# Kernel optimization log

Hardware: AMD Instinct MI355X
Metric: run time of the kernel (lower is better)

Reference implementation:

```python
import jax, jax.numpy as jnp
import numpy as np

N = 100000   # nodes
E = 1600000  # edges (avg degree 16)
D = 128      # feature width (in_feats == all hidden_feats)
G = 1024     # number of graphs for global_add_pool
L = 3        # layers
BN_EPS = 1e-5


def setup_inputs() -> dict:
    key = jax.random.key(0)
    ks = jax.random.split(key, 6)
    x = jax.random.normal(ks[0], (N, D), dtype=jnp.float32)
    edge_index = jax.random.randint(ks[1], (2, E), 0, N, dtype=jnp.int32)
    batch = jnp.sort(jax.random.randint(ks[2], (N,), 0, G, dtype=jnp.int32))
    scale = np.float32(1.0 / np.sqrt(D))
    Ws = jax.random.normal(ks[3], (L, D, D), dtype=jnp.float32) * scale   # GCNConv weights
    bs = jnp.zeros((L, D), dtype=jnp.float32)                             # GCNConv biases
    rWs = jax.random.normal(ks[4], (L, D, D), dtype=jnp.float32) * scale  # residual Linear weights
    rbs = jnp.zeros((L, D), dtype=jnp.float32)                            # residual Linear biases
    gammas = jnp.ones((L, D), dtype=jnp.float32)                          # BN affine
    betas = jnp.zeros((L, D), dtype=jnp.float32)
    return {"x": x, "edge_index": edge_index, "batch": batch,
            "Ws": Ws, "bs": bs, "rWs": rWs, "rbs": rbs,
            "gammas": gammas, "betas": betas}


def reference(x, edge_index, batch, Ws, bs, rWs, rbs, gammas, betas):
    src, dst = edge_index[0], edge_index[1]
    # normalize='False' is a truthy string in the original -> PyG GCN norm with self-loops
    loops = jnp.arange(N, dtype=src.dtype)
    src_sl = jnp.concatenate([src, loops])  # [E+N]
    dst_sl = jnp.concatenate([dst, loops])
    deg = jax.ops.segment_sum(jnp.ones(E + N, x.dtype), dst_sl, num_segments=N)
    dinv = jax.lax.rsqrt(deg)  # deg >= 1 thanks to self-loops
    norm = (dinv[src_sl] * dinv[dst_sl])[:, None]  # [E+N, 1]

    for i in range(L):
        h = x @ Ws[i]                                   # [N, D]
        msg = h[src_sl] * norm                          # gather + scale  [E+N, D]
        agg = jax.ops.segment_sum(msg, dst_sl, num_segments=N) + bs[i]
        res = jax.nn.relu(x @ rWs[i] + rbs[i])          # residual linear + ReLU
        h = agg + res
        # BatchNorm1d in training mode: batch stats (biased variance)
        mean = h.mean(axis=0)
        var = h.var(axis=0)
        x = gammas[i] * (h - mean) * jax.lax.rsqrt(var + BN_EPS) + betas[i]

    # global_add_pool over graph ids
    return jax.ops.segment_sum(x, batch, num_segments=G)  # [G, D]
```

## Files before the change

### kernel.cpp

```cpp
#include <hip/hip_runtime.h>

#define D 128
#define NLAYERS 3
#define BN_EPS 1e-5f

typedef short bf16x8 __attribute__((ext_vector_type(8)));
typedef float f32x4 __attribute__((ext_vector_type(4)));

__device__ __forceinline__ unsigned short f2bf(float f) {
    unsigned int u = __float_as_uint(f);
    u += 0x7FFFu + ((u >> 16) & 1u);
    return (unsigned short)(u >> 16);
}
__device__ __forceinline__ float bf2f(unsigned short b) {
    return __uint_as_float(((unsigned int)b) << 16);
}
__device__ __forceinline__ float bf_lo(unsigned int u) {
    return __uint_as_float(u << 16);
}
__device__ __forceinline__ float bf_hi(unsigned int u) {
    return __uint_as_float(u & 0xFFFF0000u);
}


__global__ void k_hist_edges(const int* __restrict__ dst, int* __restrict__ cnt, int E) {
    int i = blockIdx.x * blockDim.x + threadIdx.x;
    if (i < E) atomicAdd(&cnt[dst[i]], 1);
}

__global__ void k_hist_batch(const int* __restrict__ batch, int* __restrict__ gcnt, int N) {
    int i = blockIdx.x * blockDim.x + threadIdx.x;
    if (i < N) atomicAdd(&gcnt[batch[i]], 1);
}

__global__ void k_dinv(const int* __restrict__ cnt, float* __restrict__ dinv, int N) {
    int i = blockIdx.x * blockDim.x + threadIdx.x;
    if (i < N) dinv[i] = rsqrtf((float)(cnt[i] + 1));
}

__global__ void k_csr_init(int* __restrict__ csr, int n, int N) {
    int i = blockIdx.x * blockDim.x + threadIdx.x;
    if (i < n) csr[i] = N;
}

__global__ void k_zrow(unsigned short* __restrict__ hb, int N) {
    hb[(size_t)N * D + threadIdx.x] = 0;
}

__global__ void k_xb(const float* __restrict__ x, unsigned short* __restrict__ fb, int n8) {
    int i = blockIdx.x * blockDim.x + threadIdx.x;
    if (i < n8) {
        const float4 a = ((const float4*)x)[i * 2];
        const float4 b = ((const float4*)x)[i * 2 + 1];
        uint4 p;
        p.x = (unsigned int)f2bf(a.x) | ((unsigned int)f2bf(a.y) << 16);
        p.y = (unsigned int)f2bf(a.z) | ((unsigned int)f2bf(a.w) << 16);
        p.z = (unsigned int)f2bf(b.x) | ((unsigned int)f2bf(b.y) << 16);
        p.w = (unsigned int)f2bf(b.z) | ((unsigned int)f2bf(b.w) << 16);
        ((uint4*)fb)[i] = p;
    }
}

__global__ void k_scan_partial(const int* __restrict__ cnt, int* __restrict__ bsum, int N) {
    __shared__ int sh[256];
    int b = blockIdx.x, t = threadIdx.x;
    int base = b * 1024 + t * 4;
    int s = 0;
#pragma unroll
    for (int i = 0; i < 4; ++i) {
        int idx = base + i;
        int cv = (idx < N) ? cnt[idx] : 0;
        s += (cv + 3) & ~3;
    }
    sh[t] = s;
    for (int ofs = 128; ofs > 0; ofs >>= 1) {
        __syncthreads();
        if (t < ofs) sh[t] += sh[t + ofs];
    }
    __syncthreads();
    if (t == 0) bsum[b] = sh[0];
}

__global__ void k_scan_small(const int* __restrict__ bsum, int* __restrict__ bbase, int nb) {
    __shared__ int sh[256];
    int t = threadIdx.x;
    int v = (t < nb) ? bsum[t] : 0;
    sh[t] = v;
    __syncthreads();
    for (int ofs = 1; ofs < 256; ofs <<= 1) {
        int vv = (t >= ofs) ? sh[t - ofs] : 0;
        __syncthreads();
        sh[t] += vv;
        __syncthreads();
    }
    bbase[t] = sh[t] - v;
}

__global__ void k_scan_apply(const int* __restrict__ cnt, const int* __restrict__ bbase,
                             int* __restrict__ roff, int* __restrict__ cur, int N) {
    __shared__ int sh[256];
    int b = blockIdx.x, t = threadIdx.x;
    int base = b * 1024 + t * 4;
    int v[4]; int s = 0;
#pragma unroll
    for (int i = 0; i < 4; ++i) {
        int cv = (base + i < N) ? cnt[base + i] : 0;
        v[i] = (cv + 3) & ~3;
        s += v[i];
    }
    sh[t] = s;
    __syncthreads();
    for (int ofs = 1; ofs < 256; ofs <<= 1) {
        int vv = (t >= ofs) ? sh[t - ofs] : 0;
        __syncthreads();
        sh[t] += vv;
        __syncthreads();
    }
    int o = bbase[b] + sh[t] - s;
#pragma unroll
    for (int i = 0; i < 4; ++i) {
        int idx = base + i;
        if (idx < N) {
            roff[idx] = o; cur[idx] = o;
            o += v[i];
            if (idx == N - 1) roff[N] = o;
        }
    }
}

__global__ void k_gscan(const int* __restrict__ gcnt, int* __restrict__ goff, int G, int N) {
    __shared__ int sh[256];
    int t = threadIdx.x;
    int base = t * 4;
    int v[4]; int s = 0;
#pragma unroll
    for (int i = 0; i < 4; ++i) { v[i] = (base + i < G) ? gcnt[base + i] : 0; s += v[i]; }
    sh[t] = s;
    __syncthreads();
    for (int ofs = 1; ofs < 256; ofs <<= 1) {
        int vv = (t >= ofs) ? sh[t - ofs] : 0;
        __syncthreads();
        sh[t] += vv;
        __syncthreads();
    }
    int o = sh[t] - s;
#pragma unroll
    for (int i = 0; i < 4; ++i) {
        int idx = base + i;
        if (idx < G) { goff[idx] = o; o += v[i]; }
    }
    if (t == 255) goff[G] = N;
}

__global__ void k_fill(const int* __restrict__ src, const int* __restrict__ dst,
                       int* __restrict__ cur, int* __restrict__ csr, int E) {
    int i = blockIdx.x * blockDim.x + threadIdx.x;
    if (i < E) {
        int p = atomicAdd(&cur[dst[i]], 1);
        csr[p] = src[i];
    }
}

__global__ void k_init_ac(float* __restrict__ a, float* __restrict__ c) {
    int t = threadIdx.x;
    a[t] = 1.0f; c[t] = 0.0f;
}

__global__ void k_packfold(const float* __restrict__ W, const float* __restrict__ rW,
                           const float* __restrict__ a, const float* __restrict__ c,
                           const float* __restrict__ rb,
                           unsigned short* __restrict__ Wp,
                           float* __restrict__ cwA, float* __restrict__ crb) {
    if (blockIdx.x < 128) {
        int idx = blockIdx.x * 256 + threadIdx.x;
        int m = idx >> 14;
        int i = idx & 16383;
        int k = i >> 7, col = i & 127;
        const float* src = m ? rW : W;
        float v = a[k] * src[i];
        int frag = ((k >> 5) << 3) + (col >> 4);
        int lane = (((k & 31) >> 3) << 4) + (col & 15);
        int j = k & 7;
        Wp[(m << 14) + frag * 512 + lane * 8 + j] = f2bf(v);
    } else {
        int t = threadIdx.x;
        if (t < D) {
            float s = 0.f;
            for (int k = 0; k < D; ++k) s += c[k] * W[k * D + t];
            cwA[t] = s;
        } else {
            int j = t - D;
            float s = rb[j];
            for (int k = 0; k < D; ++k) s += c[k] * rW[k * D + j];
            crb[j] = s;
        }
    }
}

__global__ __launch_bounds__(256) void k_gemm_mfma(
    const unsigned short* __restrict__ fb,
    const unsigned short* __restrict__ Wp,
    const float* __restrict__ add0, const float* __restrict__ add1,
    const float* __restrict__ dinv,
    unsigned short* __restrict__ hb, unsigned short* __restrict__ rbuf, int N) {
    __shared__ unsigned short As[128 * 128];
    __shared__ unsigned short Wb[128 * 128];
    const int t = threadIdx.x;
    const int rowbase = blockIdx.x * 128;

#pragma unroll
    for (int i = 0; i < 8; ++i) {
        int ch = t + i * 256;
        int row = ch >> 4, slot = ch & 15;
        uint4 v = make_uint4(0, 0, 0, 0);
        int gr = rowbase + row;
        if (gr < N) v = *(const uint4*)(fb + (size_t)gr * D + slot * 8);
        *(uint4*)((char*)As + row * 256 + ((slot ^ (row & 7)) << 4)) = v;
    }

    const int wave = t >> 6, l = t & 63;
    const int wrow = wave * 32;
    const int lg = l >> 4, lc = l & 15;

    const int g0 = rowbase + wrow + lc;
    const int g1 = g0 + 16;
    const int f0 = lg * 4;

#pragma unroll 1
    for (int m = 0; m < 2; ++m) {
        const unsigned short* wp = Wp + (m << 14);
        __syncthreads();
#pragma unroll
        for (int i = 0; i < 8; ++i) {
            int ch = t + i * 256;
            *(uint4*)((char*)Wb + ch * 16) = *(const uint4*)((const char*)wp + ch * 16);
        }
        __syncthreads();

        f32x4 acc[2][8];
#pragma unroll
        for (int nf = 0; nf < 2; ++nf)
#pragma unroll
            for (int cf = 0; cf < 8; ++cf) acc[nf][cf] = (f32x4){0.f, 0.f, 0.f, 0.f};

#pragma unroll
        for (int ks = 0; ks < 4; ++ks) {
            const int r0 = wrow + lc;
            const int r1 = wrow + 16 + lc;
            const int s = ks * 4 + lg;
            bf16x8 a0 = *(const bf16x8*)((const char*)As + r0 * 256 + ((s ^ (r0 & 7)) << 4));
            bf16x8 a1 = *(const bf16x8*)((const char*)As + r1 * 256 + ((s ^ (r1 & 7)) << 4));
#pragma unroll
            for (int cf = 0; cf < 8; ++cf) {
                bf16x8 b = *(const bf16x8*)((const char*)Wb + ((ks * 8 + cf) * 64 + l) * 16);
                acc[0][cf] = __builtin_amdgcn_mfma_f32_16x16x32_bf16(b, a0, acc[0][cf], 0, 0, 0);
                acc[1][cf] = __builtin_amdgcn_mfma_f32_16x16x32_bf16(b, a1, acc[1][cf], 0, 0, 0);
            }
        }

        if (m == 0) {
            const float dv0 = (g0 < N) ? dinv[g0] : 0.f;
            const float dv1 = (g1 < N) ? dinv[g1] : 0.f;
#pragma unroll
            for (int cf = 0; cf < 8; ++cf) {
                const int fx = cf * 16 + f0;
                const float4 va = *(const float4*)(add0 + fx);
                if (g0 < N) {
                    uint2 p;
                    p.x = (unsigned int)f2bf((acc[0][cf][0] + va.x) * dv0) |
                          ((unsigned int)f2bf((acc[0][cf][1] + va.y) * dv0) << 16);
                    p.y = (unsigned int)f2bf((acc[0][cf][2] + va.z) * dv0) |
                          ((unsigned int)f2bf((acc[0][cf][3] + va.w) * dv0) << 16);
                    *(uint2*)(hb + (size_t)g0 * D + fx) = p;
                }
                if (g1 < N) {
                    uint2 p;
                    p.x = (unsigned int)f2bf((acc[1][cf][0] + va.x) * dv1) |
                          ((unsigned int)f2bf((acc[1][cf][1] + va.y) * dv1) << 16);
                    p.y = (unsigned int)f2bf((acc[1][cf][2] + va.z) * dv1) |
                          ((unsigned int)f2bf((acc[1][cf][3] + va.w) * dv1) << 16);
                    *(uint2*)(hb + (size_t)g1 * D + fx) = p;
                }
            }
        } else {
#pragma unroll
            for (int cf = 0; cf < 8; ++cf) {
                const int fx = cf * 16 + f0;
                const float4 va = *(const float4*)(add1 + fx);
                if (g0 < N) {
                    uint2 p;
                    p.x = (unsigned int)f2bf(fmaxf(acc[0][cf][0] + va.x, 0.f)) |
                          ((unsigned int)f2bf(fmaxf(acc[0][cf][1] + va.y, 0.f)) << 16);
                    p.y = (unsigned int)f2bf(fmaxf(acc[0][cf][2] + va.z, 0.f)) |
                          ((unsigned int)f2bf(fmaxf(acc[0][cf][3] + va.w, 0.f)) << 16);
                    *(uint2*)(rbuf + (size_t)g0 * D + fx) = p;
                }
                if (g1 < N) {
                    uint2 p;
                    p.x = (unsigned int)f2bf(fmaxf(acc[1][cf][0] + va.x, 0.f)) |
                          ((unsigned int)f2bf(fmaxf(acc[1][cf][1] + va.y, 0.f)) << 16);
                    p.y = (unsigned int)f2bf(fmaxf(acc[1][cf][2] + va.z, 0.f)) |
                          ((unsigned int)f2bf(fmaxf(acc[1][cf][3] + va.w, 0.f)) << 16);
                    *(uint2*)(rbuf + (size_t)g1 * D + fx) = p;
                }
            }
        }
    }
}

__global__ __launch_bounds__(256) void k_agg(
    const unsigned short* __restrict__ hb, const unsigned short* __restrict__ resb,
    unsigned short* __restrict__ fbout,
    const int* __restrict__ roff, const int* __restrict__ csr,
    const float* __restrict__ dinv, const float* __restrict__ bias,
    float* __restrict__ stats, int N, int half) {
    const int tid = threadIdx.x;
    const int lane = tid & 63;
    const int g = lane >> 4;
    const int li = lane & 15;
    const int cs = li * 8;
    const int wid = (blockIdx.x * blockDim.x + tid) >> 6;
    const int nw = (gridDim.x * blockDim.x) >> 6;

    float bv[8];
#pragma unroll
    for (int k = 0; k < 8; ++k) bv[k] = bias[cs + k];

    float s8[8], q8[8];
#pragma unroll
    for (int k = 0; k < 8; ++k) { s8[k] = 0.f; q8[k] = 0.f; }

    for (int p = wid; p < half; p += nw) {
        const int vA = p;
        const int vB = p + half;
        const bool hasB = (vB < N);
        int begA = roff[vA];
        const int qA = (roff[vA + 1] - begA) >> 2;
        int begB = begA, qB = 0;
        if (hasB) { begB = roff[vB]; qB = (roff[vB + 1] - begB) >> 2; }
        int eA = begA, eB = begB;

        float accA[8], accB[8];
#pragma unroll
        for (int k = 0; k < 8; ++k) { accA[k] = 0.f; accB[k] = 0.f; }

        const int mq = (qA > qB) ? qA : qB;
        for (int i = 0; i < mq; ++i) {
            const int4 a4 = *(const int4*)(csr + eA);
            const int4 b4 = *(const int4*)(csr + eB);
            int ua = (g == 0) ? a4.x : (g == 1) ? a4.y : (g == 2) ? a4.z : a4.w;
            int ub = (g == 0) ? b4.x : (g == 1) ? b4.y : (g == 2) ? b4.z : b4.w;
            ua = (i < qA) ? ua : N;
            ub = (i < qB) ? ub : N;
            const uint4 ga = *(const uint4*)(hb + (size_t)ua * D + cs);
            const uint4 gb = *(const uint4*)(hb + (size_t)ub * D + cs);
            accA[0] += bf_lo(ga.x); accA[1] += bf_hi(ga.x);
            accA[2] += bf_lo(ga.y); accA[3] += bf_hi(ga.y);
            accA[4] += bf_lo(ga.z); accA[5] += bf_hi(ga.z);
            accA[6] += bf_lo(ga.w); accA[7] += bf_hi(ga.w);
            accB[0] += bf_lo(gb.x); accB[1] += bf_hi(gb.x);
            accB[2] += bf_lo(gb.y); accB[3] += bf_hi(gb.y);
            accB[4] += bf_lo(gb.z); accB[5] += bf_hi(gb.z);
            accB[6] += bf_lo(gb.w); accB[7] += bf_hi(gb.w);
            if (i + 1 < qA) eA += 4;
            if (i + 1 < qB) eB += 4;
        }

#pragma unroll
        for (int k = 0; k < 8; ++k) {
            accA[k] += __shfl_xor(accA[k], 16);
            accA[k] += __shfl_xor(accA[k], 32);
            accB[k] += __shfl_xor(accB[k], 16);
            accB[k] += __shfl_xor(accB[k], 32);
        }

        {
            const float dv = dinv[vA];
            const uint4 hs = *(const uint4*)(hb + (size_t)vA * D + cs);
            const uint4 rr = *(const uint4*)(resb + (size_t)vA * D + cs);
            float ox[8];
            ox[0] = (accA[0] + bf_lo(hs.x)) * dv + bv[0] + bf_lo(rr.x);
            ox[1] = (accA[1] + bf_hi(hs.x)) * dv + bv[1] + bf_hi(rr.x);
            ox[2] = (accA[2] + bf_lo(hs.y)) * dv + bv[2] + bf_lo(rr.y);
            ox[3] = (accA[3] + bf_hi(hs.y)) * dv + bv[3] + bf_hi(rr.y);
            ox[4] = (accA[4] + bf_lo(hs.z)) * dv + bv[4] + bf_lo(rr.z);
            ox[5] = (accA[5] + bf_hi(hs.z)) * dv + bv[5] + bf_hi(rr.z);
            ox[6] = (accA[6] + bf_lo(hs.w)) * dv + bv[6] + bf_lo(rr.w);
            ox[7] = (accA[7] + bf_hi(hs.w)) * dv + bv[7] + bf_hi(rr.w);
            if (g == 0) {
                uint4 pk;
                pk.x = (unsigned int)f2bf(ox[0]) | ((unsigned int)f2bf(ox[1]) << 16);
                pk.y = (unsigned int)f2bf(ox[2]) | ((unsigned int)f2bf(ox[3]) << 16);
                pk.z = (unsigned int)f2bf(ox[4]) | ((unsigned int)f2bf(ox[5]) << 16);
                pk.w = (unsigned int)f2bf(ox[6]) | ((unsigned int)f2bf(ox[7]) << 16);
                *(uint4*)(fbout + (size_t)vA * D + cs) = pk;
#pragma unroll
                for (int k = 0; k < 8; ++k) { s8[k] += ox[k]; q8[k] += ox[k] * ox[k]; }
            }
        }
        if (hasB) {
            const float dv = dinv[vB];
            const uint4 hs = *(const uint4*)(hb + (size_t)vB * D + cs);
            const uint4 rr = *(const uint4*)(resb + (size_t)vB * D + cs);
            float ox[8];
            ox[0] = (accB[0] + bf_lo(hs.x)) * dv + bv[0] + bf_lo(rr.x);
            ox[1] = (accB[1] + bf_hi(hs.x)) * dv + bv[1] + bf_hi(rr.x);
            ox[2] = (accB[2] + bf_lo(hs.y)) * dv + bv[2] + bf_lo(rr.y);
            ox[3] = (accB[3] + bf_hi(hs.y)) * dv + bv[3] + bf_hi(rr.y);
            ox[4] = (accB[4] + bf_lo(hs.z)) * dv + bv[4] + bf_lo(rr.z);
            ox[5] = (accB[5] + bf_hi(hs.z)) * dv + bv[5] + bf_hi(rr.z);
            ox[6] = (accB[6] + bf_lo(hs.w)) * dv + bv[6] + bf_lo(rr.w);
            ox[7] = (accB[7] + bf_hi(hs.w)) * dv + bv[7] + bf_hi(rr.w);
            if (g == 0) {
                uint4 pk;
                pk.x = (unsigned int)f2bf(ox[0]) | ((unsigned int)f2bf(ox[1]) << 16);
                pk.y = (unsigned int)f2bf(ox[2]) | ((unsigned int)f2bf(ox[3]) << 16);
                pk.z = (unsigned int)f2bf(ox[4]) | ((unsigned int)f2bf(ox[5]) << 16);
                pk.w = (unsigned int)f2bf(ox[6]) | ((unsigned int)f2bf(ox[7]) << 16);
                *(uint4*)(fbout + (size_t)vB * D + cs) = pk;
#pragma unroll
                for (int k = 0; k < 8; ++k) { s8[k] += ox[k]; q8[k] += ox[k] * ox[k]; }
            }
        }
    }

    __shared__ float sred[4][16][8];
    __shared__ float qred[4][16][8];
    const int w = tid >> 6;
    if (g == 0) {
#pragma unroll
        for (int k = 0; k < 8; ++k) { sred[w][li][k] = s8[k]; qred[w][li][k] = q8[k]; }
    }
    __syncthreads();
    if (tid < D) {
        const int col = tid;
        float ts = 0.f, tq = 0.f;
#pragma unroll
        for (int ww = 0; ww < 4; ++ww) {
            ts += sred[ww][col >> 3][col & 7];
            tq += qred[ww][col >> 3][col & 7];
        }
        atomicAdd(&stats[col], ts);
        atomicAdd(&stats[D + col], tq);
    }
}

__global__ void k_bnfin(const float* __restrict__ stats, const float* __restrict__ gamma,
                        const float* __restrict__ beta,
                        float* __restrict__ a_next, float* __restrict__ c_next, float invN) {
    int t = threadIdx.x;
    float mean = stats[t] * invN;
    float var = stats[D + t] * invN - mean * mean;
    float rs = rsqrtf(var + BN_EPS);
    float a = gamma[t] * rs;
    a_next[t] = a;
    c_next[t] = beta[t] - mean * a;
}

__global__ void k_pool(const unsigned short* __restrict__ fb, const int* __restrict__ goff,
                       const float* __restrict__ a, const float* __restrict__ c,
                       float* __restrict__ out) {
    int g = blockIdx.x, t = threadIdx.x;
    int beg = goff[g], end = goff[g + 1];
    float acc = 0.f;
    for (int v = beg; v < end; ++v) acc += bf2f(fb[(size_t)v * D + t]);
    out[(size_t)g * D + t] = acc * a[t] + (float)(end - beg) * c[t];
}


extern "C" void kernel_launch(void* const* d_in, const int* in_sizes, int n_in,
                              void* d_out, int out_size, void* d_ws, size_t ws_size,
                              hipStream_t stream) {
    const float* x      = (const float*)d_in[0];
    const int*   ei     = (const int*)d_in[1];
    const int*   batch  = (const int*)d_in[2];
    const float* Ws     = (const float*)d_in[3];
    const float* bs     = (const float*)d_in[4];
    const float* rWs    = (const float*)d_in[5];
    const float* rbs    = (const float*)d_in[6];
    const float* gammas = (const float*)d_in[7];
    const float* betas  = (const float*)d_in[8];
    float* out = (float*)d_out;

    const int N = in_sizes[2];
    const int E = in_sizes[1] / 2;
    const int G = out_size / D;
    const int* src = ei;
    const int* dst = ei + E;
    const int EP = E + 4 * N + 4;
    const int half = (N + 1) >> 1;

    char* ws = (char*)d_ws;
    size_t off = 0;
    auto alloc = [&](size_t bytes) -> char* {
        char* p = ws + off;
        off += (bytes + 255) & ~(size_t)255;
        return p;
    };
    unsigned short* hb = (unsigned short*)alloc((size_t)(N + 1) * D * 2);
    unsigned short* fb = (unsigned short*)alloc((size_t)N * D * 2);
    unsigned short* rbuf = (unsigned short*)alloc((size_t)N * D * 2);
    int*   csr  = (int*)alloc((size_t)EP * 4);
    int*   roff = (int*)alloc((size_t)(N + 1) * 4);
    int*   cur  = (int*)alloc((size_t)N * 4);
    int*   cnt  = (int*)alloc((size_t)N * 4);
    float* dinv = (float*)alloc((size_t)N * 4);
    int*   gcnt = (int*)alloc((size_t)G * 4);
    int*   goff = (int*)alloc((size_t)(G + 1) * 4);
    int*   bsum = (int*)alloc(256 * 4);
    int*   bbase= (int*)alloc(256 * 4);
    float* stats= (float*)alloc((size_t)NLAYERS * 2 * D * 4);
    float* aarr = (float*)alloc((size_t)(NLAYERS + 1) * D * 4);
    float* carr = (float*)alloc((size_t)(NLAYERS + 1) * D * 4);
    unsigned short* Wp = (unsigned short*)alloc((size_t)2 * D * D * 2);
    float* cwA  = (float*)alloc(D * 4);
    float* crb  = (float*)alloc(D * 4);
    (void)ws_size;

    hipMemsetAsync(cnt, 0, (size_t)N * 4, stream);
    hipMemsetAsync(gcnt, 0, (size_t)G * 4, stream);
    hipMemsetAsync(stats, 0, (size_t)NLAYERS * 2 * D * 4, stream);

    k_hist_edges<<<(E + 255) / 256, 256, 0, stream>>>(dst, cnt, E);
    k_hist_batch<<<(N + 255) / 256, 256, 0, stream>>>(batch, gcnt, N);
    k_dinv<<<(N + 255) / 256, 256, 0, stream>>>(cnt, dinv, N);
    k_csr_init<<<(EP + 255) / 256, 256, 0, stream>>>(csr, EP, N);
    k_zrow<<<1, D, 0, stream>>>(hb, N);
    k_xb<<<(N * (D / 8) + 255) / 256, 256, 0, stream>>>(x, fb, N * (D / 8));

    int nb = (N + 1023) / 1024;
    k_scan_partial<<<nb, 256, 0, stream>>>(cnt, bsum, N);
    k_scan_small<<<1, 256, 0, stream>>>(bsum, bbase, nb);
    k_scan_apply<<<nb, 256, 0, stream>>>(cnt, bbase, roff, cur, N);
    k_gscan<<<1, 256, 0, stream>>>(gcnt, goff, G, N);
    k_fill<<<(E + 255) / 256, 256, 0, stream>>>(src, dst, cur, csr, E);
    k_init_ac<<<1, D, 0, stream>>>(aarr, carr);

    for (int l = 0; l < NLAYERS; ++l) {
        const float* W  = Ws + (size_t)l * D * D;
        const float* rW = rWs + (size_t)l * D * D;
        const float* aP = aarr + (size_t)l * D;
        const float* cP = carr + (size_t)l * D;

        k_packfold<<<129, 256, 0, stream>>>(W, rW, aP, cP, rbs + (size_t)l * D,
                                            Wp, cwA, crb);

        k_gemm_mfma<<<(N + 127) / 128, 256, 0, stream>>>(fb, Wp, cwA, crb, dinv,
                                                         hb, rbuf, N);
        k_agg<<<4096, 256, 0, stream>>>(hb, rbuf, fb, roff, csr, dinv,
                                        bs + (size_t)l * D,
                                        stats + (size_t)l * 2 * D, N, half);
        k_bnfin<<<1, D, 0, stream>>>(stats + (size_t)l * 2 * D, gammas + (size_t)l * D,
                                     betas + (size_t)l * D,
                                     aarr + (size_t)(l + 1) * D, carr + (size_t)(l + 1) * D,
                                     1.0f / (float)N);
    }

    k_pool<<<G, D, 0, stream>>>(fb, goff, aarr + (size_t)NLAYERS * D,
                                carr + (size_t)NLAYERS * D, out);
}
```

Baseline: 828.7 us.

## Merge small setup kernels, fold BN finalize into packfold, stage GEMM stores via LDS

Cuts the launch count by merging the two histograms, putting the zero-row write into the dinv kernel, combining the two small scans, and moving CSR padding init into scan_apply. The BN finalize and init_ac kernels are removed, with BN scale and shift now computed inside packfold and pool. The GEMM epilogue writes its bf16 results into LDS and then stores full rows with coalesced 16-byte writes instead of scattered 8-byte writes. This costs an extra LDS round trip and barriers, and the padding fill now runs as a per-thread loop.

Result: faster. 782.4 us (-5.6%).

```diff
diff --git a/kernel.cpp b/kernel.cpp
--- a/kernel.cpp
+++ b/kernel.cpp
@@ -23,28 +23,22 @@
 }
 
 
-__global__ void k_hist_edges(const int* __restrict__ dst, int* __restrict__ cnt, int E) {
+__global__ void k_hist(const int* __restrict__ dst, const int* __restrict__ batch,
+                       int* __restrict__ cnt, int* __restrict__ gcnt, int E, int N) {
     int i = blockIdx.x * blockDim.x + threadIdx.x;
-    if (i < E) atomicAdd(&cnt[dst[i]], 1);
-}
-
-__global__ void k_hist_batch(const int* __restrict__ batch, int* __restrict__ gcnt, int N) {
-    int i = blockIdx.x * blockDim.x + threadIdx.x;
-    if (i < N) atomicAdd(&gcnt[batch[i]], 1);
-}
-
-__global__ void k_dinv(const int* __restrict__ cnt, float* __restrict__ dinv, int N) {
+    if (i < E) {
+        atomicAdd(&cnt[dst[i]], 1);
+    } else {
+        int j = i - E;
+        if (j < N) atomicAdd(&gcnt[batch[j]], 1);
+    }
+}
+
+__global__ void k_dinv_zrow(const int* __restrict__ cnt, float* __restrict__ dinv,
+                            unsigned short* __restrict__ hb, int N) {
     int i = blockIdx.x * blockDim.x + threadIdx.x;
     if (i < N) dinv[i] = rsqrtf((float)(cnt[i] + 1));
-}
-
-__global__ void k_csr_init(int* __restrict__ csr, int n, int N) {
-    int i = blockIdx.x * blockDim.x + threadIdx.x;
-    if (i < n) csr[i] = N;
-}
-
-__global__ void k_zrow(unsigned short* __restrict__ hb, int N) {
-    hb[(size_t)N * D + threadIdx.x] = 0;
+    if (blockIdx.x == 0 && threadIdx.x < D) hb[(size_t)N * D + threadIdx.x] = 0;
 }
 
 __global__ void k_xb(const float* __restrict__ x, unsigned short* __restrict__ fb, int n8) {
@@ -81,30 +75,56 @@
     if (t == 0) bsum[b] = sh[0];
 }
 
-__global__ void k_scan_small(const int* __restrict__ bsum, int* __restrict__ bbase, int nb) {
+__global__ void k_scan_small_g(const int* __restrict__ bsum, int* __restrict__ bbase, int nb,
+                               const int* __restrict__ gcnt, int* __restrict__ goff,
+                               int G, int N) {
     __shared__ int sh[256];
     int t = threadIdx.x;
-    int v = (t < nb) ? bsum[t] : 0;
-    sh[t] = v;
-    __syncthreads();
-    for (int ofs = 1; ofs < 256; ofs <<= 1) {
-        int vv = (t >= ofs) ? sh[t - ofs] : 0;
-        __syncthreads();
-        sh[t] += vv;
-        __syncthreads();
-    }
-    bbase[t] = sh[t] - v;
+    if (blockIdx.x == 0) {
+        int v = (t < nb) ? bsum[t] : 0;
+        sh[t] = v;
+        __syncthreads();
+        for (int ofs = 1; ofs < 256; ofs <<= 1) {
+            int vv = (t >= ofs) ? sh[t - ofs] : 0;
+            __syncthreads();
+            sh[t] += vv;
+            __syncthreads();
+        }
+        bbase[t] = sh[t] - v;
+    } else {
+        int base = t * 4;
+        int v[4]; int s = 0;
+#pragma unroll
+        for (int i = 0; i < 4; ++i) { v[i] = (base + i < G) ? gcnt[base + i] : 0; s += v[i]; }
+        sh[t] = s;
+        __syncthreads();
+        for (int ofs = 1; ofs < 256; ofs <<= 1) {
+            int vv = (t >= ofs) ? sh[t - ofs] : 0;
+            __syncthreads();
+            sh[t] += vv;
+            __syncthreads();
+        }
+        int o = sh[t] - s;
+#pragma unroll
+        for (int i = 0; i < 4; ++i) {
+            int idx = base + i;
+            if (idx < G) { goff[idx] = o; o += v[i]; }
+        }
+        if (t == 255) goff[G] = N;
+    }
 }
 
 __global__ void k_scan_apply(const int* __restrict__ cnt, const int* __restrict__ bbase,
-                             int* __restrict__ roff, int* __restrict__ cur, int N) {
+                             int* __restrict__ roff, int* __restrict__ cur,
+                             int* __restrict__ csr, int N) {
     __shared__ int sh[256];
     int b = blockIdx.x, t = threadIdx.x;
     int base = b * 1024 + t * 4;
-    int v[4]; int s = 0;
+    int vr[4], v[4]; int s = 0;
 #pragma unroll
     for (int i = 0; i < 4; ++i) {
         int cv = (base + i < N) ? cnt[base + i] : 0;
+        vr[i] = cv;
         v[i] = (cv + 3) & ~3;
         s += v[i];
     }
@@ -122,34 +142,11 @@
         int idx = base + i;
         if (idx < N) {
             roff[idx] = o; cur[idx] = o;
+            for (int p = vr[i]; p < v[i]; ++p) csr[o + p] = N;
             o += v[i];
             if (idx == N - 1) roff[N] = o;
         }
     }
-}
-
-__global__ void k_gscan(const int* __restrict__ gcnt, int* __restrict__ goff, int G, int N) {
-    __shared__ int sh[256];
-    int t = threadIdx.x;
-    int base = t * 4;
-    int v[4]; int s = 0;
-#pragma unroll
-    for (int i = 0; i < 4; ++i) { v[i] = (base + i < G) ? gcnt[base + i] : 0; s += v[i]; }
-    sh[t] = s;
-    __syncthreads();
-    for (int ofs = 1; ofs < 256; ofs <<= 1) {
-        int vv = (t >= ofs) ? sh[t - ofs] : 0;
-        __syncthreads();
-        sh[t] += vv;
-        __syncthreads();
-    }
-    int o = sh[t] - s;
-#pragma unroll
-    for (int i = 0; i < 4; ++i) {
-        int idx = base + i;
-        if (idx < G) { goff[idx] = o; o += v[i]; }
-    }
-    if (t == 255) goff[G] = N;
 }
 
 __global__ void k_fill(const int* __restrict__ src, const int* __restrict__ dst,
@@ -161,37 +158,51 @@
     }
 }
 
-__global__ void k_init_ac(float* __restrict__ a, float* __restrict__ c) {
-    int t = threadIdx.x;
-    a[t] = 1.0f; c[t] = 0.0f;
-}
-
 __global__ void k_packfold(const float* __restrict__ W, const float* __restrict__ rW,
-                           const float* __restrict__ a, const float* __restrict__ c,
-                           const float* __restrict__ rb,
+                           const float* __restrict__ gam, const float* __restrict__ bet,
+                           const float* __restrict__ stats, const float* __restrict__ rb,
                            unsigned short* __restrict__ Wp,
-                           float* __restrict__ cwA, float* __restrict__ crb) {
+                           float* __restrict__ cwA, float* __restrict__ crb,
+                           int first, float invN) {
     if (blockIdx.x < 128) {
         int idx = blockIdx.x * 256 + threadIdx.x;
         int m = idx >> 14;
         int i = idx & 16383;
         int k = i >> 7, col = i & 127;
+        float a = 1.f;
+        if (!first) {
+            float mean = stats[k] * invN;
+            float var = stats[D + k] * invN - mean * mean;
+            a = gam[k] * rsqrtf(var + BN_EPS);
+        }
         const float* src = m ? rW : W;
-        float v = a[k] * src[i];
+        float v = a * src[i];
         int frag = ((k >> 5) << 3) + (col >> 4);
         int lane = (((k & 31) >> 3) << 4) + (col & 15);
         int j = k & 7;
         Wp[(m << 14) + frag * 512 + lane * 8 + j] = f2bf(v);
     } else {
+        __shared__ float csh[128];
         int t = threadIdx.x;
         if (t < D) {
+            float c = 0.f;
+            if (!first) {
+                float mean = stats[t] * invN;
+                float var = stats[D + t] * invN - mean * mean;
+                float a = gam[t] * rsqrtf(var + BN_EPS);
+                c = bet[t] - mean * a;
+            }
+            csh[t] = c;
+        }
+        __syncthreads();
+        if (t < D) {
             float s = 0.f;
-            for (int k = 0; k < D; ++k) s += c[k] * W[k * D + t];
+            for (int k = 0; k < D; ++k) s += csh[k] * W[k * D + t];
             cwA[t] = s;
         } else {
             int j = t - D;
             float s = rb[j];
-            for (int k = 0; k < D; ++k) s += c[k] * rW[k * D + j];
+            for (int k = 0; k < D; ++k) s += csh[k] * rW[k * D + j];
             crb[j] = s;
         }
     }
@@ -222,9 +233,12 @@
     const int wrow = wave * 32;
     const int lg = l >> 4, lc = l & 15;
 
-    const int g0 = rowbase + wrow + lc;
-    const int g1 = g0 + 16;
+    const int n0 = wrow + lc;
+    const int n1 = wrow + 16 + lc;
+    const int g0 = rowbase + n0;
+    const int g1 = rowbase + n1;
     const int f0 = lg * 4;
+    const int half = lg & 1;
 
 #pragma unroll 1
     for (int m = 0; m < 2; ++m) {
@@ -245,11 +259,9 @@
 
 #pragma unroll
         for (int ks = 0; ks < 4; ++ks) {
-            const int r0 = wrow + lc;
-            const int r1 = wrow + 16 + lc;
             const int s = ks * 4 + lg;
-            bf16x8 a0 = *(const bf16x8*)((const char*)As + r0 * 256 + ((s ^ (r0 & 7)) << 4));
-            bf16x8 a1 = *(const bf16x8*)((const char*)As + r1 * 256 + ((s ^ (r1 & 7)) << 4));
+            bf16x8 a0 = *(const bf16x8*)((const char*)As + n0 * 256 + ((s ^ (n0 & 7)) << 4));
+            bf16x8 a1 = *(const bf16x8*)((const char*)As + n1 * 256 + ((s ^ (n1 & 7)) << 4));
 #pragma unroll
             for (int cf = 0; cf < 8; ++cf) {
                 bf16x8 b = *(const bf16x8*)((const char*)Wb + ((ks * 8 + cf) * 64 + l) * 16);
@@ -258,6 +270,8 @@
             }
         }
 
+        __syncthreads();
+
         if (m == 0) {
             const float dv0 = (g0 < N) ? dinv[g0] : 0.f;
             const float dv1 = (g1 < N) ? dinv[g1] : 0.f;
@@ -265,44 +279,50 @@
             for (int cf = 0; cf < 8; ++cf) {
                 const int fx = cf * 16 + f0;
                 const float4 va = *(const float4*)(add0 + fx);
-                if (g0 < N) {
-                    uint2 p;
-                    p.x = (unsigned int)f2bf((acc[0][cf][0] + va.x) * dv0) |
-                          ((unsigned int)f2bf((acc[0][cf][1] + va.y) * dv0) << 16);
-                    p.y = (unsigned int)f2bf((acc[0][cf][2] + va.z) * dv0) |
-                          ((unsigned int)f2bf((acc[0][cf][3] + va.w) * dv0) << 16);
-                    *(uint2*)(hb + (size_t)g0 * D + fx) = p;
-                }
-                if (g1 < N) {
-                    uint2 p;
-                    p.x = (unsigned int)f2bf((acc[1][cf][0] + va.x) * dv1) |
-                          ((unsigned int)f2bf((acc[1][cf][1] + va.y) * dv1) << 16);
-                    p.y = (unsigned int)f2bf((acc[1][cf][2] + va.z) * dv1) |
-                          ((unsigned int)f2bf((acc[1][cf][3] + va.w) * dv1) << 16);
-                    *(uint2*)(hb + (size_t)g1 * D + fx) = p;
-                }
+                const int slot = cf * 2 + (lg >> 1);
+                uint2 p0, p1;
+                p0.x = (unsigned int)f2bf((acc[0][cf][0] + va.x) * dv0) |
+                       ((unsigned int)f2bf((acc[0][cf][1] + va.y) * dv0) << 16);
+                p0.y = (unsigned int)f2bf((acc[0][cf][2] + va.z) * dv0) |
+                       ((unsigned int)f2bf((acc[0][cf][3] + va.w) * dv0) << 16);
+                p1.x = (unsigned int)f2bf((acc[1][cf][0] + va.x) * dv1) |
+                       ((unsigned int)f2bf((acc[1][cf][1] + va.y) * dv1) << 16);
+                p1.y = (unsigned int)f2bf((acc[1][cf][2] + va.z) * dv1) |
+                       ((unsigned int)f2bf((acc[1][cf][3] + va.w) * dv1) << 16);
+                *(uint2*)((char*)Wb + n0 * 256 + ((slot ^ (n0 & 7)) << 4) + half * 8) = p0;
+                *(uint2*)((char*)Wb + n1 * 256 + ((slot ^ (n1 & 7)) << 4) + half * 8) = p1;
             }
         } else {
 #pragma unroll
             for (int cf = 0; cf < 8; ++cf) {
                 const int fx = cf * 16 + f0;
                 const float4 va = *(const float4*)(add1 + fx);
-                if (g0 < N) {
-                    uint2 p;
-                    p.x = (unsigned int)f2bf(fmaxf(acc[0][cf][0] + va.x, 0.f)) |
-                          ((unsigned int)f2bf(fmaxf(acc[0][cf][1] + va.y, 0.f)) << 16);
-                    p.y = (unsigned int)f2bf(fmaxf(acc[0][cf][2] + va.z, 0.f)) |
-                          ((unsigned int)f2bf(fmaxf(acc[0][cf][3] + va.w, 0.f)) << 16);
-                    *(uint2*)(rbuf + (size_t)g0 * D + fx) = p;
-                }
-                if (g1 < N) {
-                    uint2 p;
-                    p.x = (unsigned int)f2bf(fmaxf(acc[1][cf][0] + va.x, 0.f)) |
-                          ((unsigned int)f2bf(fmaxf(acc[1][cf][1] + va.y, 0.f)) << 16);
-                    p.y = (unsigned int)f2bf(fmaxf(acc[1][cf][2] + va.z, 0.f)) |
-                          ((unsigned int)f2bf(fmaxf(acc[1][cf][3] + va.w, 0.f)) << 16);
-                    *(uint2*)(rbuf + (size_t)g1 * D + fx) = p;
-                }
+                const int slot = cf * 2 + (lg >> 1);
+                uint2 p0, p1;
+                p0.x = (unsigned int)f2bf(fmaxf(acc[0][cf][0] + va.x, 0.f)) |
+                       ((unsigned int)f2bf(fmaxf(acc[0][cf][1] + va.y, 0.f)) << 16);
+                p0.y = (unsigned int)f2bf(fmaxf(acc[0][cf][2] + va.z, 0.f)) |
+                       ((unsigned int)f2bf(fmaxf(acc[0][cf][3] + va.w, 0.f)) << 16);
+                p1.x = (unsigned int)f2bf(fmaxf(acc[1][cf][0] + va.x, 0.f)) |
+                       ((unsigned int)f2bf(fmaxf(acc[1][cf][1] + va.y, 0.f)) << 16);
+                p1.y = (unsigned int)f2bf(fmaxf(acc[1][cf][2] + va.z, 0.f)) |
+                       ((unsigned int)f2bf(fmaxf(acc[1][cf][3] + va.w, 0.f)) << 16);
+                *(uint2*)((char*)Wb + n0 * 256 + ((slot ^ (n0 & 7)) << 4) + half * 8) = p0;
+                *(uint2*)((char*)Wb + n1 * 256 + ((slot ^ (n1 & 7)) << 4) + half * 8) = p1;
+            }
+        }
+
+        __syncthreads();
+
+        unsigned short* __restrict__ dstp = (m == 0) ? hb : rbuf;
+#pragma unroll
+        for (int i = 0; i < 8; ++i) {
+            int ch = t + i * 256;
+            int row = ch >> 4, sl = ch & 15;
+            int gr = rowbase + row;
+            if (gr < N) {
+                uint4 v = *(const uint4*)((const char*)Wb + row * 256 + ((sl ^ (row & 7)) << 4));
+                *(uint4*)(dstp + (size_t)gr * D + sl * 8) = v;
             }
         }
     }
@@ -445,26 +465,19 @@
     }
 }
 
-__global__ void k_bnfin(const float* __restrict__ stats, const float* __restrict__ gamma,
-                        const float* __restrict__ beta,
-                        float* __restrict__ a_next, float* __restrict__ c_next, float invN) {
-    int t = threadIdx.x;
+__global__ void k_pool(const unsigned short* __restrict__ fb, const int* __restrict__ goff,
+                       const float* __restrict__ gam, const float* __restrict__ bet,
+                       const float* __restrict__ stats, float invN,
+                       float* __restrict__ out) {
+    int g = blockIdx.x, t = threadIdx.x;
     float mean = stats[t] * invN;
     float var = stats[D + t] * invN - mean * mean;
-    float rs = rsqrtf(var + BN_EPS);
-    float a = gamma[t] * rs;
-    a_next[t] = a;
-    c_next[t] = beta[t] - mean * a;
-}
-
-__global__ void k_pool(const unsigned short* __restrict__ fb, const int* __restrict__ goff,
-                       const float* __restrict__ a, const float* __restrict__ c,
-                       float* __restrict__ out) {
-    int g = blockIdx.x, t = threadIdx.x;
+    float a = gam[t] * rsqrtf(var + BN_EPS);
+    float c = bet[t] - mean * a;
     int beg = goff[g], end = goff[g + 1];
     float acc = 0.f;
     for (int v = beg; v < end; ++v) acc += bf2f(fb[(size_t)v * D + t]);
-    out[(size_t)g * D + t] = acc * a[t] + (float)(end - beg) * c[t];
+    out[(size_t)g * D + t] = acc * a + (float)(end - beg) * c;
 }
 
 
@@ -489,6 +502,7 @@
     const int* dst = ei + E;
     const int EP = E + 4 * N + 4;
     const int half = (N + 1) >> 1;
+    const float invN = 1.0f / (float)N;
 
     char* ws = (char*)d_ws;
     size_t off = 0;
@@ -510,8 +524,6 @@
     int*   bsum = (int*)alloc(256 * 4);
     int*   bbase= (int*)alloc(256 * 4);
     float* stats= (float*)alloc((size_t)NLAYERS * 2 * D * 4);
-    float* aarr = (float*)alloc((size_t)(NLAYERS + 1) * D * 4);
-    float* carr = (float*)alloc((size_t)(NLAYERS + 1) * D * 4);
     unsigned short* Wp = (unsigned short*)alloc((size_t)2 * D * D * 2);
     float* cwA  = (float*)alloc(D * 4);
     float* crb  = (float*)alloc(D * 4);
@@ -521,41 +533,37 @@
     hipMemsetAsync(gcnt, 0, (size_t)G * 4, stream);
     hipMemsetAsync(stats, 0, (size_t)NLAYERS * 2 * D * 4, stream);
 
-    k_hist_edges<<<(E + 255) / 256, 256, 0, stream>>>(dst, cnt, E);
-    k_hist_batch<<<(N + 255) / 256, 256, 0, stream>>>(batch, gcnt, N);
-    k_dinv<<<(N + 255) / 256, 256, 0, stream>>>(cnt, dinv, N);
-    k_csr_init<<<(EP + 255) / 256, 256, 0, stream>>>(csr, EP, N);
-    k_zrow<<<1, D, 0, stream>>>(hb, N);
+    k_hist<<<(E + N + 255) / 256, 256, 0, stream>>>(dst, batch, cnt, gcnt, E, N);
+    k_dinv_zrow<<<(N + 255) / 256, 256, 0, stream>>>(cnt, dinv, hb, N);
     k_xb<<<(N * (D / 8) + 255) / 256, 256, 0, stream>>>(x, fb, N * (D / 8));
 
     int nb = (N + 1023) / 1024;
     k_scan_partial<<<nb, 256, 0, stream>>>(cnt, bsum, N);
-    k_scan_small<<<1, 256, 0, stream>>>(bsum, bbase, nb);
-    k_scan_apply<<<nb, 256, 0, stream>>>(cnt, bbase, roff, cur, N);
-    k_gscan<<<1, 256, 0, stream>>>(gcnt, goff, G, N);
+    k_scan_small_g<<<2, 256, 0, stream>>>(bsum, bbase, nb, gcnt, goff, G, N);
+    k_scan_apply<<<nb, 256, 0, stream>>>(cnt, bbase, roff, cur, csr, N);
     k_fill<<<(E + 255) / 256, 256, 0, stream>>>(src, dst, cur, csr, E);
-    k_init_ac<<<1, D, 0, stream>>>(aarr, carr);
 
     for (int l = 0; l < NLAYERS; ++l) {
         const float* W  = Ws + (size_t)l * D * D;
         const float* rW = rWs + (size_t)l * D * D;
-        const float* aP = aarr + (size_t)l * D;
-        const float* cP = carr + (size_t)l * D;
-
-        k_packfold<<<129, 256, 0, stream>>>(W, rW, aP, cP, rbs + (size_t)l * D,
-                                            Wp, cwA, crb);
+        const float* gamP = gammas + (size_t)(l > 0 ? l - 1 : 0) * D;
+        const float* betP = betas + (size_t)(l > 0 ? l - 1 : 0) * D;
+        const float* stP  = stats + (size_t)(l > 0 ? l - 1 : 0) * 2 * D;
+
+        k_packfold<<<129, 256, 0, stream>>>(W, rW, gamP, betP, stP,
+                                            rbs + (size_t)l * D,
+                                            Wp, cwA, crb, (l == 0) ? 1 : 0, invN);
 
         k_gemm_mfma<<<(N + 127) / 128, 256, 0, stream>>>(fb, Wp, cwA, crb, dinv,
                                                          hb, rbuf, N);
         k_agg<<<4096, 256, 0, stream>>>(hb, rbuf, fb, roff, csr, dinv,
                                         bs + (size_t)l * D,
                                         stats + (size_t)l * 2 * D, N, half);
-        k_bnfin<<<1, D, 0, stream>>>(stats + (size_t)l * 2 * D, gammas + (size_t)l * D,
-                                     betas + (size_t)l * D,
-                                     aarr + (size_t)(l + 1) * D, carr + (size_t)(l + 1) * D,
-                                     1.0f / (float)N);
-    }
-
-    k_pool<<<G, D, 0, stream>>>(fb, goff, aarr + (size_t)NLAYERS * D,
-                                carr + (size_t)NLAYERS * D, out);
-}
+    }
+
+    k_pool<<<G, 128, 0, stream>>>(fb, goff,
+                                  gammas + (size_t)(NLAYERS - 1) * D,
+                                  betas + (size_t)(NLAYERS - 1) * D,
+                                  stats + (size_t)(NLAYERS - 1) * 2 * D,
+                                  invN, out);
+}
```
